# Kernel tuning notes

Measured on AMD Instinct MI355X. Metric: run time of the kernel, lower is better.

The kernel has to match this reference:

```python
import jax, jax.numpy as jnp
import numpy as np

N = 50000      # nodes
E = 800000     # edges
D_IN = 128
D_OUT = 128
R = 8          # relation types
EPS = 1e-12    # F.normalize eps


def setup_inputs() -> dict:
    key = jax.random.key(0)
    ks = jax.random.split(key, 10)
    s_in = 1.0 / np.sqrt(D_IN)
    s_out = 1.0 / np.sqrt(D_OUT)
    return {
        "x": jax.random.normal(ks[0], (N, D_IN), jnp.float32),
        "W1": jax.random.normal(ks[1], (R, D_IN, D_OUT), jnp.float32) * s_in,
        "loopW1": jax.random.normal(ks[2], (D_IN, D_OUT), jnp.float32) * s_in,
        "b1": jax.random.normal(ks[3], (D_OUT,), jnp.float32) * 0.01,
        "W2": jax.random.normal(ks[4], (R, D_OUT, D_OUT), jnp.float32) * s_out,
        "loopW2": jax.random.normal(ks[5], (D_OUT, D_OUT), jnp.float32) * s_out,
        "b2": jax.random.normal(ks[6], (D_OUT,), jnp.float32) * 0.01,
        "src": jax.random.randint(ks[7], (E,), 0, N),
        "dst": jax.random.randint(ks[8], (E,), 0, N),
        "etypes": jax.random.randint(ks[9], (E,), 0, R),
    }


def rel_layer(x, src, dst, etypes, W, loopW, b):
    # transform every node by every relation: [R, N, D_out]
    xw = jnp.einsum('ni,rio->rno', x, W)
    # gather per-edge messages: [E, D_out]
    msg = xw[etypes, src]
    # scatter-add to destination nodes
    agg = jax.ops.segment_sum(msg, dst, num_segments=x.shape[0])
    # self-loop + bias (DGL RelGraphConv defaults)
    return agg + x @ loopW + b


def reference(x, W1, loopW1, b1, W2, loopW2, b2, src, dst, etypes):
    h = jax.nn.relu(rel_layer(x, src, dst, etypes, W1, loopW1, b1))
    h = rel_layer(h, src, dst, etypes, W2, loopW2, b2)
    # F.normalize: row-wise L2, eps=1e-12
    nrm = jnp.maximum(jnp.linalg.norm(h, axis=1, keepdims=True), EPS)
    return h / nrm
```

## Files before the change

kernel.cpp:

```cpp
#include <hip/hip_runtime.h>
#include <hip/hip_bf16.h>

#define D 128

typedef unsigned int u32;
typedef unsigned short u16;
typedef __attribute__((ext_vector_type(8))) short s16x8;
typedef __attribute__((ext_vector_type(4))) float f32x4;
typedef __attribute__((ext_vector_type(2))) float f32x2;

__device__ __forceinline__ float bf2f(u16 u) {
    union { u32 u; float f; } v; v.u = ((u32)u) << 16; return v.f;
}
__device__ __forceinline__ u16 f2bf(float f) {
    union { float f; u32 u; } v; v.f = f;
    return (u16)((v.u + 0x7fffu + ((v.u >> 16) & 1u)) >> 16);
}
__device__ __forceinline__ u32 pack_bf2(float a, float b) {
    __hip_bfloat162 t = __float22bfloat162_rn(make_float2(a, b));
    union { __hip_bfloat162 t; u32 u; } v; v.t = t; return v.u;
}
__device__ __forceinline__ void unpack2(u32 u, float& lo, float& hi) {
    union { u32 u; float f; } a, b;
    a.u = u << 16; b.u = u & 0xffff0000u;
    lo = a.f; hi = b.f;
}

__global__ void detect_dtype(const u16* __restrict__ x, int* __restrict__ flag) {
    __shared__ int cnt;
    if (threadIdx.x == 0) cnt = 0;
    __syncthreads();
    u16 u = x[2 * threadIdx.x];
    int e = (u >> 7) & 0xFF;
    if (e >= 96 && e <= 150) atomicAdd(&cnt, 1);
    __syncthreads();
    if (threadIdx.x == 0) *flag = (cnt >= 128) ? 0 : 1;
}

__global__ __launch_bounds__(256)
void to_bf16_all(const void* __restrict__ s0, const void* __restrict__ s1,
                 const void* __restrict__ s2, const void* __restrict__ s3,
                 const void* __restrict__ s4, const void* __restrict__ s5,
                 const void* __restrict__ s6,
                 u16* __restrict__ d0, u16* __restrict__ d1, u16* __restrict__ d2,
                 u16* __restrict__ d3, u16* __restrict__ d4, u16* __restrict__ d5,
                 u16* __restrict__ d6,
                 long long n0, long long n1, long long n2, long long n3,
                 long long n4, long long n5, long long n6,
                 const int* __restrict__ flag)
{
    long long i = (long long)blockIdx.x * 256 + threadIdx.x;
    const void* s; u16* d; long long off;
    if      (i < n0)                               { s = s0; d = d0; off = i; }
    else if (i < n0+n1)                            { s = s1; d = d1; off = i-n0; }
    else if (i < n0+n1+n2)                         { s = s2; d = d2; off = i-n0-n1; }
    else if (i < n0+n1+n2+n3)                      { s = s3; d = d3; off = i-n0-n1-n2; }
    else if (i < n0+n1+n2+n3+n4)                   { s = s4; d = d4; off = i-n0-n1-n2-n3; }
    else if (i < n0+n1+n2+n3+n4+n5)                { s = s5; d = d5; off = i-n0-n1-n2-n3-n4; }
    else if (i < n0+n1+n2+n3+n4+n5+n6)             { s = s6; d = d6; off = i-n0-n1-n2-n3-n4-n5; }
    else return;
    if (*flag) d[off] = f2bf(((const float*)s)[off]);
    else       d[off] = ((const u16*)s)[off];
}

__global__ __launch_bounds__(256)
void zero_ints(int* __restrict__ a, int n) {
    int i = blockIdx.x * 256 + threadIdx.x;
    if (i < n) a[i] = 0;
}

__global__ __launch_bounds__(256)
void hist(const int* __restrict__ dst, int* __restrict__ counts, int E) {
    int e = blockIdx.x * 256 + threadIdx.x;
    if (e < E) atomicAdd(&counts[dst[e]], 1);
}

__global__ __launch_bounds__(256)
void scan_p1(const int* __restrict__ in, int* __restrict__ offs, int* __restrict__ bsum, int n) {
    __shared__ int wpart[4];
    int b = blockIdx.x, tid = threadIdx.x;
    int i = b * 256 + tid, lane = tid & 63, wid = tid >> 6;
    int v = (i < n) ? in[i] : 0;
    int s = v;
#pragma unroll
    for (int off = 1; off < 64; off <<= 1) {
        int t = __shfl_up(s, off, 64);
        if (lane >= off) s += t;
    }
    if (lane == 63) wpart[wid] = s;
    __syncthreads();
    int add = 0;
    for (int w = 0; w < wid; ++w) add += wpart[w];
    if (i < n) offs[i] = add + s - v;
    if (tid == 255) bsum[b] = add + s;
}

__global__ __launch_bounds__(1024)
void scan_p2(int* __restrict__ bsum, int* __restrict__ offs, int nb, int N_) {
    __shared__ int wpart[16];
    int tid = threadIdx.x, lane = tid & 63, wid = tid >> 6;
    int v = (tid < nb) ? bsum[tid] : 0;
    int s = v;
#pragma unroll
    for (int off = 1; off < 64; off <<= 1) {
        int t = __shfl_up(s, off, 64);
        if (lane >= off) s += t;
    }
    if (lane == 63) wpart[wid] = s;
    __syncthreads();
    int add = 0;
    for (int w = 0; w < wid; ++w) add += wpart[w];
    int excl = add + s - v;
    __syncthreads();
    if (tid < nb) bsum[tid] = excl;
    if (tid == nb - 1) offs[N_] = excl + v;
}

__global__ __launch_bounds__(256)
void scan_p3(int* __restrict__ offs, const int* __restrict__ bsum, int n) {
    int i = blockIdx.x * 256 + threadIdx.x;
    if (i < n) offs[i] += bsum[blockIdx.x];
}

__global__ __launch_bounds__(256)
void copy_ints(const int* __restrict__ in, int* __restrict__ out, int n) {
    int i = blockIdx.x * 256 + threadIdx.x;
    if (i < n) out[i] = in[i];
}

__global__ __launch_bounds__(256)
void fill_csr(const int* __restrict__ src, const int* __restrict__ dst,
              const int* __restrict__ et, int* __restrict__ cursor,
              int* __restrict__ rowidx, int E, int N) {
    int e = blockIdx.x * 256 + threadIdx.x;
    if (e >= E) return;
    int p = atomicAdd(&cursor[dst[e]], 1);
    rowidx[p] = et[e] * N + src[e];
}

__global__ __launch_bounds__(256)
void gemm_k128(const u16* __restrict__ A, const u16* __restrict__ W,
               const u16* __restrict__ loopW, const u16* __restrict__ bias,
               int M, int R_, u16* __restrict__ xw, u16* __restrict__ sl)
{
    __shared__ u16 As[128 * 128];
    const int y = blockIdx.y;
    const u16* B = (y < R_) ? (W + (long long)y * D * D) : loopW;
    const int row0 = blockIdx.x * 128;
    const int tid  = threadIdx.x;
    const int lane = tid & 63;
    const int wv   = tid >> 6;
    const int quad = lane >> 4;
    const int l16  = lane & 15;

    {
        int r_base = (wv << 2) + (lane >> 4);
        int c      = lane & 15;
        auto* lds0 = (__attribute__((address_space(3))) char*)As;
#pragma unroll
        for (int it = 0; it < 8; ++it) {
            int rl = it * 16 + r_base;
            int cg = c ^ (rl & 15);
            int rg = row0 + rl; if (rg >= M) rg = M - 1;
            const u16* gp = A + (long long)rg * D + cg * 8;
            __builtin_amdgcn_global_load_lds(
                (const __attribute__((address_space(1))) void*)gp,
                (__attribute__((address_space(3))) void*)(lds0 + it * 4096 + wv * 1024),
                16, 0, 0);
        }
    }

    s16x8 bf[4][2];
#pragma unroll
    for (int kk = 0; kk < 4; ++kk)
#pragma unroll
        for (int j = 0; j < 8; ++j) {
            u32 p = *(const u32*)(B + (kk * 32 + quad * 8 + j) * D + wv * 32 + 2 * l16);
            bf[kk][0][j] = (short)(p & 0xffffu);
            bf[kk][1][j] = (short)(p >> 16);
        }

    f32x4 acc[8][2];
#pragma unroll
    for (int mt = 0; mt < 8; ++mt) { acc[mt][0] = (f32x4)0.f; acc[mt][1] = (f32x4)0.f; }

    __syncthreads();

#pragma unroll
    for (int kk = 0; kk < 4; ++kk) {
        const int chunk = (kk * 4 + quad) ^ l16;
#pragma unroll
        for (int mt = 0; mt < 8; ++mt) {
            int rl = mt * 16 + l16;
            s16x8 a = *(const s16x8*)(As + rl * D + chunk * 8);
            acc[mt][0] = __builtin_amdgcn_mfma_f32_16x16x32_bf16(a, bf[kk][0], acc[mt][0], 0, 0, 0);
            acc[mt][1] = __builtin_amdgcn_mfma_f32_16x16x32_bf16(a, bf[kk][1], acc[mt][1], 0, 0, 0);
        }
    }

    long long MD64 = (long long)M * 64;
    int cpair = wv * 16 + l16;
    if (y < R_) {
        u32* o = (u32*)xw + (long long)y * MD64;
#pragma unroll
        for (int mt = 0; mt < 8; ++mt)
#pragma unroll
            for (int i = 0; i < 4; ++i) {
                int r = row0 + mt * 16 + quad * 4 + i;
                if (r >= M) continue;
                o[(long long)r * 64 + cpair] = pack_bf2(acc[mt][0][i], acc[mt][1][i]);
            }
    } else {
        float b0 = bf2f(bias[wv * 32 + 2 * l16]);
        float b1 = bf2f(bias[wv * 32 + 2 * l16 + 1]);
        u32* o = (u32*)sl;
#pragma unroll
        for (int mt = 0; mt < 8; ++mt)
#pragma unroll
            for (int i = 0; i < 4; ++i) {
                int r = row0 + mt * 16 + quad * 4 + i;
                if (r >= M) continue;
                o[(long long)r * 64 + cpair] = pack_bf2(acc[mt][0][i] + b0, acc[mt][1][i] + b1);
            }
    }
}

__global__ __launch_bounds__(256)
void aggregate(const u16* __restrict__ xw, const u16* __restrict__ sl,
               const int* __restrict__ offs, const int* __restrict__ rowidx,
               void* __restrict__ out, int N, int mode, const int* __restrict__ flag)
{
    int node = blockIdx.x * 4 + (threadIdx.x >> 6);
    int p = threadIdx.x & 63;
    if (node >= N) return;
    const u32* xw32 = (const u32*)xw;

    float a0, a1;
    unpack2(((const u32*)sl)[(long long)node * 64 + p], a0, a1);

    int j = offs[node], end = offs[node + 1];
    for (; j + 4 <= end; j += 4) {
        int r0 = rowidx[j], r1 = rowidx[j + 1], r2 = rowidx[j + 2], r3 = rowidx[j + 3];
        u32 u0 = xw32[(long long)r0 * 64 + p];
        u32 u1 = xw32[(long long)r1 * 64 + p];
        u32 u2 = xw32[(long long)r2 * 64 + p];
        u32 u3 = xw32[(long long)r3 * 64 + p];
        float l, h;
        unpack2(u0, l, h); a0 += l; a1 += h;
        unpack2(u1, l, h); a0 += l; a1 += h;
        unpack2(u2, l, h); a0 += l; a1 += h;
        unpack2(u3, l, h); a0 += l; a1 += h;
    }
    for (; j < end; ++j) {
        float l, h;
        unpack2(xw32[(long long)rowidx[j] * 64 + p], l, h);
        a0 += l; a1 += h;
    }

    if (mode == 0) {
        a0 = fmaxf(a0, 0.f); a1 = fmaxf(a1, 0.f);
        ((u32*)out)[(long long)node * 64 + p] = pack_bf2(a0, a1);
    } else {
        float s = a0 * a0 + a1 * a1;
#pragma unroll
        for (int off = 32; off > 0; off >>= 1) s += __shfl_xor(s, off, 64);
        float sc = 1.f / fmaxf(sqrtf(s), 1e-12f);
        a0 *= sc; a1 *= sc;
        if (*flag) {
            f32x2 w; w[0] = a0; w[1] = a1;
            ((f32x2*)out)[(long long)node * 64 + p] = w;
        } else {
            ((u32*)out)[(long long)node * 64 + p] = pack_bf2(a0, a1);
        }
    }
}

static inline size_t align256(size_t x) { return (x + 255) & ~(size_t)255; }

extern "C" void kernel_launch(void* const* d_in, const int* in_sizes, int n_in,
                              void* d_out, int out_size, void* d_ws, size_t ws_size,
                              hipStream_t stream)
{
    const void* x_in   = d_in[0];
    const void* W1_in  = d_in[1];
    const void* lW1_in = d_in[2];
    const void* b1_in  = d_in[3];
    const void* W2_in  = d_in[4];
    const void* lW2_in = d_in[5];
    const void* b2_in  = d_in[6];
    const int* src = (const int*)d_in[7];
    const int* dst = (const int*)d_in[8];
    const int* et  = (const int*)d_in[9];

    const int N = in_sizes[0] / D;
    const int E = in_sizes[7];
    const int R = in_sizes[1] / (D * D);

    const long long ND  = (long long)N * D;
    const long long RDD = (long long)R * D * D;
    const long long DDl = (long long)D * D;

    size_t off = 0;
    auto alloc = [&](size_t bytes) { size_t o = off; off = align256(off + bytes); return o; };
    size_t o_flag = alloc(256);
    size_t o_xc   = alloc((size_t)ND * 2);
    size_t o_W1   = alloc((size_t)RDD * 2);
    size_t o_lW1  = alloc((size_t)DDl * 2);
    size_t o_b1   = alloc((size_t)D * 2);
    size_t o_W2   = alloc((size_t)RDD * 2);
    size_t o_lW2  = alloc((size_t)DDl * 2);
    size_t o_b2   = alloc((size_t)D * 2);
    size_t o_sl   = alloc((size_t)ND * 2);
    size_t o_h    = alloc((size_t)ND * 2);
    size_t o_offs = alloc((size_t)(N + 1) * 4);
    size_t o_cur  = alloc((size_t)(N + 1) * 4);
    size_t o_bsum = alloc(4096);
    size_t o_ridx = alloc((size_t)E * 4);
    size_t o_xw   = alloc((size_t)R * ND * 2);
    (void)ws_size;

    char* ws = (char*)d_ws;
    int* flag   = (int*)(ws + o_flag);
    u16* x_c    = (u16*)(ws + o_xc);
    u16* W1c    = (u16*)(ws + o_W1);
    u16* lW1c   = (u16*)(ws + o_lW1);
    u16* b1c    = (u16*)(ws + o_b1);
    u16* W2c    = (u16*)(ws + o_W2);
    u16* lW2c   = (u16*)(ws + o_lW2);
    u16* b2c    = (u16*)(ws + o_b2);
    u16* sl     = (u16*)(ws + o_sl);
    u16* h      = (u16*)(ws + o_h);
    int* offs   = (int*)(ws + o_offs);
    int* cursor = (int*)(ws + o_cur);
    int* bsum   = (int*)(ws + o_bsum);
    int* rowidx = (int*)(ws + o_ridx);
    u16* xw     = (u16*)(ws + o_xw);

    dim3 blk(256, 1, 1);
    int mb = (N + 127) / 128;
    int nb = (N + 255) / 256;
    auto cdiv = [](long long n) { return (u32)((n + 255) / 256); };

    detect_dtype<<<dim3(1), blk, 0, stream>>>((const u16*)x_in, flag);
    long long tot = ND + RDD + DDl + D + RDD + DDl + D;
    to_bf16_all<<<dim3(cdiv(tot)), blk, 0, stream>>>(
        x_in, W1_in, lW1_in, b1_in, W2_in, lW2_in, b2_in,
        x_c, W1c, lW1c, b1c, W2c, lW2c, b2c,
        ND, RDD, DDl, (long long)D, RDD, DDl, (long long)D, flag);

    zero_ints<<<dim3(cdiv(N)), blk, 0, stream>>>(cursor, N);
    hist<<<dim3(cdiv(E)), blk, 0, stream>>>(dst, cursor, E);
    scan_p1<<<dim3(nb), blk, 0, stream>>>(cursor, offs, bsum, N);
    scan_p2<<<dim3(1), dim3(1024), 0, stream>>>(bsum, offs, nb, N);
    scan_p3<<<dim3(nb), blk, 0, stream>>>(offs, bsum, N);
    copy_ints<<<dim3(cdiv(N)), blk, 0, stream>>>(offs, cursor, N);
    fill_csr<<<dim3(cdiv(E)), blk, 0, stream>>>(src, dst, et, cursor, rowidx, E, N);

    gemm_k128<<<dim3(mb, R + 1), blk, 0, stream>>>(x_c, W1c, lW1c, b1c, N, R, xw, sl);
    aggregate<<<dim3((N + 3) / 4), blk, 0, stream>>>(xw, sl, offs, rowidx, h, N, 0, flag);

    gemm_k128<<<dim3(mb, R + 1), blk, 0, stream>>>(h, W2c, lW2c, b2c, N, R, xw, sl);
    aggregate<<<dim3((N + 3) / 4), blk, 0, stream>>>(xw, sl, offs, rowidx, d_out, N, 1, flag);
}
```

Baseline: 341.1 us.

## Build CSR by two-level bucket partition and skip bf16 copy when unnecessary

Replaces the global per-node atomic histogram, three-pass scan and atomic fill with a two-level counting sort. Edges are first bucketed by dst>>8 using shared-memory counts and then laid out node-by-node within each bucket, so most atomics stay in LDS and the launch count drops. The dtype conversion kernel now returns early when inputs are already bf16, and the GEMM reads the original buffers through the flag instead of a copy. This adds an extra E-sized staging buffer and packs the local node id into 8 bits, which requires et*N+src to fit in 24 bits.

```diff
diff --git a/kernel.cpp b/kernel.cpp
--- a/kernel.cpp
+++ b/kernel.cpp
@@ -2,6 +2,7 @@
 #include <hip/hip_bf16.h>
 
 #define D 128
+#define CH 4096
 
 typedef unsigned int u32;
 typedef unsigned short u16;
@@ -49,18 +50,18 @@
                  long long n4, long long n5, long long n6,
                  const int* __restrict__ flag)
 {
+    if (*flag == 0) return;
     long long i = (long long)blockIdx.x * 256 + threadIdx.x;
     const void* s; u16* d; long long off;
-    if      (i < n0)                               { s = s0; d = d0; off = i; }
-    else if (i < n0+n1)                            { s = s1; d = d1; off = i-n0; }
-    else if (i < n0+n1+n2)                         { s = s2; d = d2; off = i-n0-n1; }
-    else if (i < n0+n1+n2+n3)                      { s = s3; d = d3; off = i-n0-n1-n2; }
-    else if (i < n0+n1+n2+n3+n4)                   { s = s4; d = d4; off = i-n0-n1-n2-n3; }
-    else if (i < n0+n1+n2+n3+n4+n5)                { s = s5; d = d5; off = i-n0-n1-n2-n3-n4; }
-    else if (i < n0+n1+n2+n3+n4+n5+n6)             { s = s6; d = d6; off = i-n0-n1-n2-n3-n4-n5; }
+    if      (i < n0)                   { s = s0; d = d0; off = i; }
+    else if (i < n0+n1)                { s = s1; d = d1; off = i-n0; }
+    else if (i < n0+n1+n2)             { s = s2; d = d2; off = i-n0-n1; }
+    else if (i < n0+n1+n2+n3)          { s = s3; d = d3; off = i-n0-n1-n2; }
+    else if (i < n0+n1+n2+n3+n4)       { s = s4; d = d4; off = i-n0-n1-n2-n3; }
+    else if (i < n0+n1+n2+n3+n4+n5)    { s = s5; d = d5; off = i-n0-n1-n2-n3-n4; }
+    else if (i < n0+n1+n2+n3+n4+n5+n6) { s = s6; d = d6; off = i-n0-n1-n2-n3-n4-n5; }
     else return;
-    if (*flag) d[off] = f2bf(((const float*)s)[off]);
-    else       d[off] = ((const u16*)s)[off];
+    d[off] = f2bf(((const float*)s)[off]);
 }
 
 __global__ __launch_bounds__(256)
@@ -70,17 +71,27 @@
 }
 
 __global__ __launch_bounds__(256)
-void hist(const int* __restrict__ dst, int* __restrict__ counts, int E) {
-    int e = blockIdx.x * 256 + threadIdx.x;
-    if (e < E) atomicAdd(&counts[dst[e]], 1);
-}
-
-__global__ __launch_bounds__(256)
-void scan_p1(const int* __restrict__ in, int* __restrict__ offs, int* __restrict__ bsum, int n) {
+void csr_count(const int* __restrict__ dst, int* __restrict__ gcnt, int E, int nbuck) {
+    __shared__ int scnt[256];
+    int tid = threadIdx.x;
+    scnt[tid] = 0;
+    __syncthreads();
+    int base = blockIdx.x * CH;
+#pragma unroll
+    for (int it = 0; it < CH / 256; ++it) {
+        int e = base + it * 256 + tid;
+        if (e < E) atomicAdd(&scnt[dst[e] >> 8], 1);
+    }
+    __syncthreads();
+    if (tid < nbuck && scnt[tid] > 0) atomicAdd(&gcnt[tid], scnt[tid]);
+}
+
+__global__ __launch_bounds__(256)
+void csr_scan(const int* __restrict__ gcnt, int* __restrict__ bstart, int* __restrict__ bcur,
+              int nbuck, int N_, int E_, int* __restrict__ offs) {
     __shared__ int wpart[4];
-    int b = blockIdx.x, tid = threadIdx.x;
-    int i = b * 256 + tid, lane = tid & 63, wid = tid >> 6;
-    int v = (i < n) ? in[i] : 0;
+    int tid = threadIdx.x, lane = tid & 63, wid = tid >> 6;
+    int v = (tid < nbuck) ? gcnt[tid] : 0;
     int s = v;
 #pragma unroll
     for (int off = 1; off < 64; off <<= 1) {
@@ -91,16 +102,58 @@
     __syncthreads();
     int add = 0;
     for (int w = 0; w < wid; ++w) add += wpart[w];
-    if (i < n) offs[i] = add + s - v;
-    if (tid == 255) bsum[b] = add + s;
-}
-
-__global__ __launch_bounds__(1024)
-void scan_p2(int* __restrict__ bsum, int* __restrict__ offs, int nb, int N_) {
-    __shared__ int wpart[16];
-    int tid = threadIdx.x, lane = tid & 63, wid = tid >> 6;
-    int v = (tid < nb) ? bsum[tid] : 0;
-    int s = v;
+    int excl = add + s - v;
+    if (tid <= nbuck) bstart[tid] = excl;
+    if (tid < nbuck)  bcur[tid]  = excl;
+    if (tid == 0) offs[N_] = E_;
+}
+
+__global__ __launch_bounds__(256)
+void csr_part(const int* __restrict__ src, const int* __restrict__ dst,
+              const int* __restrict__ et, int* __restrict__ bcur,
+              u32* __restrict__ ebuf, int E, int N, int nbuck) {
+    __shared__ int scnt[256], sbase[256];
+    int tid = threadIdx.x;
+    scnt[tid] = 0;
+    __syncthreads();
+    int base = blockIdx.x * CH;
+#pragma unroll
+    for (int it = 0; it < CH / 256; ++it) {
+        int e = base + it * 256 + tid;
+        if (e < E) atomicAdd(&scnt[dst[e] >> 8], 1);
+    }
+    __syncthreads();
+    if (tid < nbuck) {
+        int c = scnt[tid];
+        sbase[tid] = c ? atomicAdd(&bcur[tid], c) : 0;
+    }
+    __syncthreads();
+    scnt[tid] = 0;
+    __syncthreads();
+#pragma unroll
+    for (int it = 0; it < CH / 256; ++it) {
+        int e = base + it * 256 + tid;
+        if (e >= E) continue;
+        int d = dst[e];
+        int b = d >> 8;
+        int p = sbase[b] + atomicAdd(&scnt[b], 1);
+        ebuf[p] = ((u32)(d & 255) << 24) | (u32)(et[e] * N + src[e]);
+    }
+}
+
+__global__ __launch_bounds__(256)
+void csr_emit(const u32* __restrict__ ebuf, const int* __restrict__ bstart,
+              int* __restrict__ offs, int* __restrict__ rowidx, int N) {
+    __shared__ int hist[256], excl[256], cur[256];
+    __shared__ int wpart[4];
+    int b = blockIdx.x, tid = threadIdx.x;
+    int lo = bstart[b], hi = bstart[b + 1];
+    hist[tid] = 0; cur[tid] = 0;
+    __syncthreads();
+    for (int i = lo + tid; i < hi; i += 256) atomicAdd(&hist[ebuf[i] >> 24], 1);
+    __syncthreads();
+    int lane = tid & 63, wid = tid >> 6;
+    int v = hist[tid], s = v;
 #pragma unroll
     for (int off = 1; off < 64; off <<= 1) {
         int t = __shfl_up(s, off, 64);
@@ -110,42 +163,36 @@
     __syncthreads();
     int add = 0;
     for (int w = 0; w < wid; ++w) add += wpart[w];
-    int excl = add + s - v;
-    __syncthreads();
-    if (tid < nb) bsum[tid] = excl;
-    if (tid == nb - 1) offs[N_] = excl + v;
-}
-
-__global__ __launch_bounds__(256)
-void scan_p3(int* __restrict__ offs, const int* __restrict__ bsum, int n) {
-    int i = blockIdx.x * 256 + threadIdx.x;
-    if (i < n) offs[i] += bsum[blockIdx.x];
-}
-
-__global__ __launch_bounds__(256)
-void copy_ints(const int* __restrict__ in, int* __restrict__ out, int n) {
-    int i = blockIdx.x * 256 + threadIdx.x;
-    if (i < n) out[i] = in[i];
-}
-
-__global__ __launch_bounds__(256)
-void fill_csr(const int* __restrict__ src, const int* __restrict__ dst,
-              const int* __restrict__ et, int* __restrict__ cursor,
-              int* __restrict__ rowidx, int E, int N) {
-    int e = blockIdx.x * 256 + threadIdx.x;
-    if (e >= E) return;
-    int p = atomicAdd(&cursor[dst[e]], 1);
-    rowidx[p] = et[e] * N + src[e];
-}
-
-__global__ __launch_bounds__(256)
-void gemm_k128(const u16* __restrict__ A, const u16* __restrict__ W,
-               const u16* __restrict__ loopW, const u16* __restrict__ bias,
+    int e_ = add + s - v;
+    excl[tid] = e_;
+    int node = (b << 8) + tid;
+    if (node < N) offs[node] = lo + e_;
+    __syncthreads();
+    for (int i = lo + tid; i < hi; i += 256) {
+        u32 rec = ebuf[i];
+        int dl = rec >> 24;
+        int p = lo + excl[dl] + atomicAdd(&cur[dl], 1);
+        rowidx[p] = (int)(rec & 0xFFFFFFu);
+    }
+}
+
+__global__ __launch_bounds__(256)
+void gemm_k128(const u16* __restrict__ Ac, const u16* __restrict__ Ao,
+               const u16* __restrict__ Wc, const u16* __restrict__ Wo,
+               const u16* __restrict__ lWc, const u16* __restrict__ lWo,
+               const u16* __restrict__ bc, const u16* __restrict__ bo,
+               const int* __restrict__ flag,
                int M, int R_, u16* __restrict__ xw, u16* __restrict__ sl)
 {
     __shared__ u16 As[128 * 128];
+    const bool f = (*flag != 0);
+    const u16* A     = f ? Ac  : Ao;
+    const u16* Wall  = f ? Wc  : Wo;
+    const u16* loopW = f ? lWc : lWo;
+    const u16* bias  = f ? bc  : bo;
+
     const int y = blockIdx.y;
-    const u16* B = (y < R_) ? (W + (long long)y * D * D) : loopW;
+    const u16* B = (y < R_) ? (Wall + (long long)y * D * D) : loopW;
     const int row0 = blockIdx.x * 128;
     const int tid  = threadIdx.x;
     const int lane = tid & 63;
@@ -295,6 +342,7 @@
     const int N = in_sizes[0] / D;
     const int E = in_sizes[7];
     const int R = in_sizes[1] / (D * D);
+    const int nbuck = (N + 255) >> 8;
 
     const long long ND  = (long long)N * D;
     const long long RDD = (long long)R * D * D;
@@ -313,8 +361,10 @@
     size_t o_sl   = alloc((size_t)ND * 2);
     size_t o_h    = alloc((size_t)ND * 2);
     size_t o_offs = alloc((size_t)(N + 1) * 4);
-    size_t o_cur  = alloc((size_t)(N + 1) * 4);
-    size_t o_bsum = alloc(4096);
+    size_t o_gcnt = alloc(1024);
+    size_t o_bst  = alloc(1040 * 4);
+    size_t o_bcur = alloc(1024);
+    size_t o_ebuf = alloc((size_t)E * 4);
     size_t o_ridx = alloc((size_t)E * 4);
     size_t o_xw   = alloc((size_t)R * ND * 2);
     (void)ws_size;
@@ -331,14 +381,16 @@
     u16* sl     = (u16*)(ws + o_sl);
     u16* h      = (u16*)(ws + o_h);
     int* offs   = (int*)(ws + o_offs);
-    int* cursor = (int*)(ws + o_cur);
-    int* bsum   = (int*)(ws + o_bsum);
+    int* gcnt   = (int*)(ws + o_gcnt);
+    int* bstart = (int*)(ws + o_bst);
+    int* bcur   = (int*)(ws + o_bcur);
+    u32* ebuf   = (u32*)(ws + o_ebuf);
     int* rowidx = (int*)(ws + o_ridx);
     u16* xw     = (u16*)(ws + o_xw);
 
     dim3 blk(256, 1, 1);
-    int mb = (N + 127) / 128;
-    int nb = (N + 255) / 256;
+    int mb   = (N + 127) / 128;
+    int nblkE = (E + CH - 1) / CH;
     auto cdiv = [](long long n) { return (u32)((n + 255) / 256); };
 
     detect_dtype<<<dim3(1), blk, 0, stream>>>((const u16*)x_in, flag);
@@ -348,17 +400,19 @@
         x_c, W1c, lW1c, b1c, W2c, lW2c, b2c,
         ND, RDD, DDl, (long long)D, RDD, DDl, (long long)D, flag);
 
-    zero_ints<<<dim3(cdiv(N)), blk, 0, stream>>>(cursor, N);
-    hist<<<dim3(cdiv(E)), blk, 0, stream>>>(dst, cursor, E);
-    scan_p1<<<dim3(nb), blk, 0, stream>>>(cursor, offs, bsum, N);
-    scan_p2<<<dim3(1), dim3(1024), 0, stream>>>(bsum, offs, nb, N);
-    scan_p3<<<dim3(nb), blk, 0, stream>>>(offs, bsum, N);
-    copy_ints<<<dim3(cdiv(N)), blk, 0, stream>>>(offs, cursor, N);
-    fill_csr<<<dim3(cdiv(E)), blk, 0, stream>>>(src, dst, et, cursor, rowidx, E, N);
-
-    gemm_k128<<<dim3(mb, R + 1), blk, 0, stream>>>(x_c, W1c, lW1c, b1c, N, R, xw, sl);
+    zero_ints<<<dim3(1), blk, 0, stream>>>(gcnt, nbuck);
+    csr_count<<<dim3(nblkE), blk, 0, stream>>>(dst, gcnt, E, nbuck);
+    csr_scan<<<dim3(1), blk, 0, stream>>>(gcnt, bstart, bcur, nbuck, N, E, offs);
+    csr_part<<<dim3(nblkE), blk, 0, stream>>>(src, dst, et, bcur, ebuf, E, N, nbuck);
+    csr_emit<<<dim3(nbuck), blk, 0, stream>>>(ebuf, bstart, offs, rowidx, N);
+
+    gemm_k128<<<dim3(mb, R + 1), blk, 0, stream>>>(
+        x_c, (const u16*)x_in, W1c, (const u16*)W1_in, lW1c, (const u16*)lW1_in,
+        b1c, (const u16*)b1_in, flag, N, R, xw, sl);
     aggregate<<<dim3((N + 3) / 4), blk, 0, stream>>>(xw, sl, offs, rowidx, h, N, 0, flag);
 
-    gemm_k128<<<dim3(mb, R + 1), blk, 0, stream>>>(h, W2c, lW2c, b2c, N, R, xw, sl);
+    gemm_k128<<<dim3(mb, R + 1), blk, 0, stream>>>(
+        h, h, W2c, (const u16*)W2_in, lW2c, (const u16*)lW2_in,
+        b2c, (const u16*)b2_in, flag, N, R, xw, sl);
     aggregate<<<dim3((N + 3) / 4), blk, 0, stream>>>(xw, sl, offs, rowidx, d_out, N, 1, flag);
 }
```

After: 303.6 us. 11.0% less time.
